# Optimization experiments

Hardware: AMD Instinct MI355X
Metric: run time of the kernel (lower is better)

## Reference

```python
import jax, jax.numpy as jnp
import numpy as np


def setup_inputs() -> dict:
    key = jax.random.key(0)
    ks = jax.random.split(key, 6)
    B, S, H = 4, 256, 768            # batch, subword seq len, BERT hidden
    N = 128                          # token_num (word-level units)
    HID, L = 1024, 16                # MLP hidden, label count
    all_hidden = jax.random.normal(ks[0], (B, S, H), dtype=jnp.float32)
    starts = jax.random.randint(ks[1], (B, N), 0, S)
    W1 = jax.random.normal(ks[2], (4 * H, HID), dtype=jnp.float32) * 0.02
    b1 = jnp.zeros((HID,), dtype=jnp.float32)
    W2 = jax.random.normal(ks[3], (HID, L), dtype=jnp.float32) * 0.02
    b2 = jnp.zeros((L,), dtype=jnp.float32)
    return {"all_hidden": all_hidden, "starts": starts,
            "W1": W1, "b1": b1, "W2": W2, "b2": b2}


def reference(all_hidden, starts, W1, b1, W2, b2):
    # Span gather: con_repr[b, n, :] = all_hidden[b, starts[b, n], :]
    con = jnp.take_along_axis(all_hidden, starts[:, :, None], axis=1)  # [B, N, H]
    B, N, H = con.shape
    a = jnp.broadcast_to(con[:, :, None, :], (B, N, N, H))  # ext_row
    c = jnp.broadcast_to(con[:, None, :, :], (B, N, N, H))  # ext_column
    table = jnp.concatenate([a, c, a - c, a * c], axis=-1)   # [B, N, N, 4H]
    hid = jnp.tanh(jnp.einsum('bijf,fh->bijh', table, W1) + b1)
    out = jnp.einsum('bijh,hl->bijl', hid, W2) + b2          # [B, N, N, L]
    return out
```

## Files before the change

kernel.cpp:

```cpp
#include <hip/hip_runtime.h>
#include <hip/hip_bf16.h>

typedef __attribute__((ext_vector_type(8))) short short8;
typedef __attribute__((ext_vector_type(8))) unsigned short ushort8;
typedef __attribute__((ext_vector_type(4))) float floatx4;
typedef __attribute__((ext_vector_type(16))) float floatx16;
typedef __attribute__((ext_vector_type(4))) unsigned int uint4v;
typedef __attribute__((ext_vector_type(2))) unsigned int uint2v;

#define DEVINL static __device__ __forceinline__

DEVINL float b2f(unsigned short s){ union{unsigned u; float f;} v; v.u=((unsigned)s)<<16; return v.f; }
DEVINL unsigned fbits(float f){ union{float f; unsigned u;} v; v.f=f; return v.u; }
DEVINL unsigned pack2(float f0, float f1){
  return __builtin_amdgcn_perm(fbits(f1)+0x8000u, fbits(f0)+0x8000u, 0x07060302u);
}
DEVINL unsigned cvt_pk(float lo, float hi){
  unsigned r;
  asm("v_cvt_pk_bf16_f32 %0, %1, %2" : "=v"(r) : "v"(lo), "v"(hi));
  return r;
}
DEVINL float tanh_fast(float v){
  float ex = __builtin_amdgcn_exp2f(v * 2.885390081777927f);
  return 1.f - 2.f*__builtin_amdgcn_rcpf(1.f + ex);
}

constexpr int Sc=256, Hc=768, Nc=128, HIDc=1024, Lc=16;

__global__ __launch_bounds__(256) void k_prep(const float* __restrict__ AH,
                                              const int* __restrict__ ST,
                                              const float* __restrict__ W1,
                                              const float* __restrict__ W2,
                                              unsigned short* __restrict__ con,
                                              unsigned short* __restrict__ w1mF,
                                              unsigned short* __restrict__ w2F2,
                                              unsigned short* __restrict__ wPQF){
  int bid = blockIdx.x, t = threadIdx.x;
  if (bid < 512) {
    int row = bid;
    int b = row >> 7;
    int st = ST[row];
    const float* src = AH + ((size_t)(b*Sc + st))*Hc;
    unsigned short* dst = con + (size_t)row*Hc;
    if (t < 192) {
      float4 v = reinterpret_cast<const float4*>(src)[t];
      uint2v o = { pack2(v.x, v.y), pack2(v.z, v.w) };
      *reinterpret_cast<uint2v*>(dst + 4*t) = o;
    }
  } else if (bid < 896) {
    int sid = (bid - 512)*256 + t;
    int l = sid & 63, kc = (sid >> 6) % 48, ht = sid / (48*64);
    int k = kc*16 + (l >> 5)*8;
    int h = ht*32 + (l & 31);
    const float* wp = W1 + (size_t)(2304 + k)*1024 + h;
    uint4v d;
    d[0] = pack2(wp[0],      wp[1024]);
    d[1] = pack2(wp[2*1024], wp[3*1024]);
    d[2] = pack2(wp[4*1024], wp[5*1024]);
    d[3] = pack2(wp[6*1024], wp[7*1024]);
    *reinterpret_cast<uint4v*>(w1mF + (size_t)sid*8) = d;
  } else if (bid < 912) {
    int gid = (bid - 896)*256 + t;
    int l = gid & 63, chunk = gid >> 6;
    int row = l & 31, s = l >> 5;
    unsigned u[4];
    #pragma unroll
    for (int p = 0; p < 4; ++p) {
      int e0 = 2*p, e1 = 2*p + 1;
      int h0 = chunk*16 + 4*s + (e0 & 3) + 8*(e0 >> 2);
      int h1 = chunk*16 + 4*s + (e1 & 3) + 8*(e1 >> 2);
      float v0 = (row < 16) ? W2[(size_t)h0*Lc + row] : 0.f;
      float v1 = (row < 16) ? W2[(size_t)h1*Lc + row] : 0.f;
      u[p] = pack2(v0, v1);
    }
    uint4v d = { u[0], u[1], u[2], u[3] };
    *reinterpret_cast<uint4v*>(w2F2 + (size_t)gid*8) = d;
  } else {
    int sid = (bid - 912)*256 + t;
    int lane = sid & 63, kcq = (sid >> 6) % 24, ht = sid / (24*64);
    int col = lane & 15, seg = lane >> 4;
    int hp = ht*16 + col;
    int kb = kcq*32 + seg*8;
    uint4v d;
    if (hp < 1024) {
      const float* w0 = W1 + (size_t)kb*1024 + hp;
      const float* wd = W1 + (size_t)(1536+kb)*1024 + hp;
      d[0] = pack2(w0[0]+wd[0],           w0[1024]+wd[1024]);
      d[1] = pack2(w0[2*1024]+wd[2*1024], w0[3*1024]+wd[3*1024]);
      d[2] = pack2(w0[4*1024]+wd[4*1024], w0[5*1024]+wd[5*1024]);
      d[3] = pack2(w0[6*1024]+wd[6*1024], w0[7*1024]+wd[7*1024]);
    } else {
      int hq = hp - 1024;
      const float* wc = W1 + (size_t)(768+kb)*1024 + hq;
      const float* wd = W1 + (size_t)(1536+kb)*1024 + hq;
      d[0] = pack2(wc[0]-wd[0],           wc[1024]-wd[1024]);
      d[1] = pack2(wc[2*1024]-wd[2*1024], wc[3*1024]-wd[3*1024]);
      d[2] = pack2(wc[4*1024]-wd[4*1024], wc[5*1024]-wd[5*1024]);
      d[3] = pack2(wc[6*1024]-wd[6*1024], wc[7*1024]-wd[7*1024]);
    }
    *reinterpret_cast<uint4v*>(wPQF + (size_t)sid*8) = d;
  }
}

__global__ __launch_bounds__(256) void k_pq(const unsigned short* __restrict__ con,
                                            const unsigned short* __restrict__ wPQF,
                                            float* __restrict__ P, float* __restrict__ Q){
  int rg = blockIdx.x >> 4, hg = blockIdx.x & 15;
  int t = threadIdx.x, w = t >> 6, lane = t & 63;
  int colh = lane & 15, rseg = lane >> 4;
  floatx4 zero = {0.f,0.f,0.f,0.f};
  floatx4 acc[2][2] = {{zero,zero},{zero,zero}};
  const unsigned short* a0p = con + (size_t)(rg*32 + colh)*Hc + rseg*8;
  const unsigned short* a1p = a0p + 16*Hc;
  const unsigned short* b0p = wPQF + (((size_t)((hg*8 + w*2)*24)) << 9) + (lane << 3);
  const unsigned short* b1p = b0p + (24 << 9);
  #pragma unroll
  for (int kc = 0; kc < 24; ++kc) {
    short8 af0 = *reinterpret_cast<const short8*>(a0p + kc*32);
    short8 af1 = *reinterpret_cast<const short8*>(a1p + kc*32);
    short8 bf0 = *reinterpret_cast<const short8*>(b0p + ((size_t)kc << 9));
    short8 bf1 = *reinterpret_cast<const short8*>(b1p + ((size_t)kc << 9));
    acc[0][0] = __builtin_amdgcn_mfma_f32_16x16x32_bf16(af0, bf0, acc[0][0], 0,0,0);
    acc[0][1] = __builtin_amdgcn_mfma_f32_16x16x32_bf16(af0, bf1, acc[0][1], 0,0,0);
    acc[1][0] = __builtin_amdgcn_mfma_f32_16x16x32_bf16(af1, bf0, acc[1][0], 0,0,0);
    acc[1][1] = __builtin_amdgcn_mfma_f32_16x16x32_bf16(af1, bf1, acc[1][1], 0,0,0);
  }
  #pragma unroll
  for (int m = 0; m < 2; ++m)
    #pragma unroll
    for (int n = 0; n < 2; ++n)
      #pragma unroll
      for (int rr = 0; rr < 4; ++rr) {
        int row = rg*32 + m*16 + rseg*4 + rr;
        int hp = hg*128 + w*32 + n*16 + colh;
        float val = acc[m][n][rr];
        if (hg < 8) P[(size_t)row*HIDc + hp] = val;
        else        Q[(size_t)row*HIDc + (hp - 1024)] = val;
      }
}

__global__ __launch_bounds__(512, 2) void k_main(const unsigned short* __restrict__ con,
    const unsigned short* __restrict__ w1mF, const unsigned short* __restrict__ w2F2,
    const float* __restrict__ P, const float* __restrict__ Q, const float* __restrict__ b1,
    const float* __restrict__ b2v, float* __restrict__ out){
  __shared__ __align__(16) unsigned short conF[2*48*64*8];
  __shared__ float Pi_lds[1024];

  int bid = blockIdx.x;
  int xcd = bid & 7, i = bid >> 3;
  int b = xcd >> 1, jh = xcd & 1;
  int bi = b*128 + i, bN = b*128;
  int t = threadIdx.x, w = t >> 6, lane = t & 63;
  int col32 = lane & 31, hi5 = lane >> 5;

  if (t < 256) {
    float4 p4 = reinterpret_cast<const float4*>(P + (size_t)(bN + i)*HIDc)[t];
    float4 b4 = reinterpret_cast<const float4*>(b1)[t];
    float4 s4 = { p4.x + b4.x, p4.y + b4.y, p4.z + b4.z, p4.w + b4.w };
    *reinterpret_cast<float4*>(&Pi_lds[4*t]) = s4;
  }
  {
    const unsigned short* conI = con + (size_t)(bN + i)*Hc;
    #pragma unroll
    for (int r = 0; r < 12; ++r) {
      int s = r*512 + t;
      int jt = (s >= 3072) ? 1 : 0;
      int rem = s - jt*3072;
      int kc = rem >> 6, ln = rem & 63;
      int j = jh*64 + jt*32 + (ln & 31);
      int kb = kc*16 + ((ln >> 5) << 3);
      ushort8 c8 = *reinterpret_cast<const ushort8*>(con + (size_t)(bN + j)*Hc + kb);
      ushort8 a8 = *reinterpret_cast<const ushort8*>(conI + kb);
      uint4v d;
      d[0] = cvt_pk(b2f(a8[0])*b2f(c8[0]), b2f(a8[1])*b2f(c8[1]));
      d[1] = cvt_pk(b2f(a8[2])*b2f(c8[2]), b2f(a8[3])*b2f(c8[3]));
      d[2] = cvt_pk(b2f(a8[4])*b2f(c8[4]), b2f(a8[5])*b2f(c8[5]));
      d[3] = cvt_pk(b2f(a8[6])*b2f(c8[6]), b2f(a8[7])*b2f(c8[7]));
      *reinterpret_cast<uint4v*>(conF + (size_t)s*8) = d;
    }
  }
  __syncthreads();

  const unsigned short* wp = w1mF + (((size_t)(w*4)*48) << 9) + (lane << 3);
  const unsigned short* yb = conF + (lane << 3);
  constexpr size_t HTS = (size_t)48 << 9;
  constexpr size_t KCS = (size_t)1 << 9;
  constexpr size_t JTS = (size_t)48 << 9;

  floatx16 a0j0, a0j1, a1j0, a1j1, a2j0, a2j1, a3j0, a3j1;
  #pragma unroll
  for (int r = 0; r < 16; ++r) {
    a0j0[r]=0.f; a0j1[r]=0.f; a1j0[r]=0.f; a1j1[r]=0.f;
    a2j0[r]=0.f; a2j1[r]=0.f; a3j0[r]=0.f; a3j1[r]=0.f;
  }

#define LOADSET(W0,W1,W2,W3,Y0,Y1, KC) { \
  W0 = *reinterpret_cast<const ushort8*>(wp + (0*HTS) + (size_t)(KC)*KCS); \
  W1 = *reinterpret_cast<const ushort8*>(wp + (1*HTS) + (size_t)(KC)*KCS); \
  W2 = *reinterpret_cast<const ushort8*>(wp + (2*HTS) + (size_t)(KC)*KCS); \
  W3 = *reinterpret_cast<const ushort8*>(wp + (3*HTS) + (size_t)(KC)*KCS); \
  Y0 = *reinterpret_cast<const short8*>(yb + (size_t)(KC)*KCS); \
  Y1 = *reinterpret_cast<const short8*>(yb + JTS + (size_t)(KC)*KCS); }

#define MFMA8S(W0,W1,W2,W3,Y0,Y1) { \
  a0j0 = __builtin_amdgcn_mfma_f32_32x32x16_bf16(W0, Y0, a0j0, 0,0,0); \
  a0j1 = __builtin_amdgcn_mfma_f32_32x32x16_bf16(W0, Y1, a0j1, 0,0,0); \
  a1j0 = __builtin_amdgcn_mfma_f32_32x32x16_bf16(W1, Y0, a1j0, 0,0,0); \
  a1j1 = __builtin_amdgcn_mfma_f32_32x32x16_bf16(W1, Y1, a1j1, 0,0,0); \
  a2j0 = __builtin_amdgcn_mfma_f32_32x32x16_bf16(W2, Y0, a2j0, 0,0,0); \
  a2j1 = __builtin_amdgcn_mfma_f32_32x32x16_bf16(W2, Y1, a2j1, 0,0,0); \
  a3j0 = __builtin_amdgcn_mfma_f32_32x32x16_bf16(W3, Y0, a3j0, 0,0,0); \
  a3j1 = __builtin_amdgcn_mfma_f32_32x32x16_bf16(W3, Y1, a3j1, 0,0,0); }

  {
    ushort8 wA0,wA1,wA2,wA3, wB0,wB1,wB2,wB3;
    short8 yA0,yA1, yB0,yB1;
    LOADSET(wA0,wA1,wA2,wA3,yA0,yA1, 0);
    #pragma unroll
    for (int kp = 0; kp < 24; ++kp) {
      LOADSET(wB0,wB1,wB2,wB3,yB0,yB1, 2*kp+1);
      MFMA8S(wA0,wA1,wA2,wA3,yA0,yA1);
      if (kp < 23) LOADSET(wA0,wA1,wA2,wA3,yA0,yA1, 2*kp+2);
      MFMA8S(wB0,wB1,wB2,wB3,yB0,yB1);
    }
  }
#undef LOADSET
#undef MFMA8S

  floatx16 acc2_0, acc2_1;
  #pragma unroll
  for (int r = 0; r < 16; ++r) { acc2_0[r] = 0.f; acc2_1[r] = 0.f; }

#define EPI(M, AJ0, AJ1) { \
  int htg = w*4 + (M); \
  const unsigned short* w2p = w2F2 + (((size_t)(htg*2)) << 9) + (lane << 3); \
  ushort8 wf0 = *reinterpret_cast<const ushort8*>(w2p); \
  ushort8 wf1 = *reinterpret_cast<const ushort8*>(w2p + 512); \
  int hbase = htg*32 + 4*hi5; \
  _Pragma("unroll") \
  for (int jt = 0; jt < 2; ++jt) { \
    const floatx16& a = (jt==0) ? AJ0 : AJ1; \
    floatx16& a2 = (jt==0) ? acc2_0 : acc2_1; \
    const float* qrow = Q + (size_t)(bN + jh*64 + jt*32 + col32)*HIDc + hbase; \
    unsigned hfu[2][4]; \
    _Pragma("unroll") \
    for (int q = 0; q < 4; ++q) { \
      floatx4 qv = *reinterpret_cast<const floatx4*>(qrow + 8*q); \
      floatx4 pf = *reinterpret_cast<const floatx4*>(&Pi_lds[hbase + 8*q]); \
      float t0 = tanh_fast(a[q*4+0] + pf[0] + qv[0]); \
      float t1 = tanh_fast(a[q*4+1] + pf[1] + qv[1]); \
      float t2 = tanh_fast(a[q*4+2] + pf[2] + qv[2]); \
      float t3 = tanh_fast(a[q*4+3] + pf[3] + qv[3]); \
      hfu[q >> 1][(q & 1)*2 + 0] = cvt_pk(t0, t1); \
      hfu[q >> 1][(q & 1)*2 + 1] = cvt_pk(t2, t3); \
    } \
    union { uint4v u; short8 s; } f0, f1; \
    f0.u[0]=hfu[0][0]; f0.u[1]=hfu[0][1]; f0.u[2]=hfu[0][2]; f0.u[3]=hfu[0][3]; \
    f1.u[0]=hfu[1][0]; f1.u[1]=hfu[1][1]; f1.u[2]=hfu[1][2]; f1.u[3]=hfu[1][3]; \
    a2 = __builtin_amdgcn_mfma_f32_32x32x16_bf16(wf0, f0.s, a2, 0,0,0); \
    a2 = __builtin_amdgcn_mfma_f32_32x32x16_bf16(wf1, f1.s, a2, 0,0,0); \
  } }

  EPI(0, a0j0, a0j1);
  EPI(1, a1j0, a1j1);
  EPI(2, a2j0, a2j1);
  EPI(3, a3j0, a3j1);
#undef EPI

  __syncthreads();
  float* red = reinterpret_cast<float*>(conF);
  #pragma unroll
  for (int q = 0; q < 2; ++q) {
    floatx4 v0 = { acc2_0[q*4+0], acc2_0[q*4+1], acc2_0[q*4+2], acc2_0[q*4+3] };
    floatx4 v1 = { acc2_1[q*4+0], acc2_1[q*4+1], acc2_1[q*4+2], acc2_1[q*4+3] };
    *reinterpret_cast<floatx4*>(&red[((w*4 + 0*2 + q)*64 + lane)*4]) = v0;
    *reinterpret_cast<floatx4*>(&red[((w*4 + 1*2 + q)*64 + lane)*4]) = v1;
  }
  __syncthreads();
  if (w < 4) {
    int jtR = w & 1, qR = w >> 1;
    floatx4 s = {0.f,0.f,0.f,0.f};
    #pragma unroll
    for (int src = 0; src < 8; ++src) {
      floatx4 v = *reinterpret_cast<const floatx4*>(&red[((src*4 + jtR*2 + qR)*64 + lane)*4]);
      s[0]+=v[0]; s[1]+=v[1]; s[2]+=v[2]; s[3]+=v[3];
    }
    int jout = jh*64 + jtR*32 + col32;
    int Lb = 8*qR + 4*hi5;
    float* op = out + ((size_t)bi*Nc + jout)*Lc + Lb;
    #pragma unroll
    for (int c = 0; c < 4; ++c) op[c] = s[c] + b2v[Lb + c];
  }
}

extern "C" void kernel_launch(void* const* d_in, const int* in_sizes, int n_in,
                              void* d_out, int out_size, void* d_ws, size_t ws_size,
                              hipStream_t stream) {
  const float* AH = (const float*)d_in[0];
  const int*   ST = (const int*)d_in[1];
  const float* W1 = (const float*)d_in[2];
  const float* b1 = (const float*)d_in[3];
  const float* W2 = (const float*)d_in[4];
  const float* b2 = (const float*)d_in[5];
  float* out = (float*)d_out;

  char* ws = (char*)d_ws;
  unsigned short* con  = (unsigned short*)ws;
  unsigned short* w1mF = (unsigned short*)(ws +   786432);
  unsigned short* wPQF = (unsigned short*)(ws +  2359296);
  float* P = (float*)(ws + 5505024);
  float* Q = (float*)(ws + 7602176);
  unsigned short* w2F2 = (unsigned short*)(ws + 9699328);

  k_prep<<<1680, 256, 0, stream>>>(AH, ST, W1, W2, con, w1mF, w2F2, wPQF);
  k_pq<<<256, 256, 0, stream>>>(con, wPQF, P, Q);
  k_main<<<1024, 512, 0, stream>>>(con, w1mF, w2F2, P, Q, b1, b2, out);
}
```

Baseline: 151.7 us.

## Stream W1 tiles into LDS via async global_load_lds double buffering

Replaces the register-prefetched global loads of the W1 fragments in the main GEMM loop with direct global-to-LDS async loads into a per-wave double-buffered LDS ring, gated by vmcnt waits and setprio around the MFMA block. The bias b1 is folded into P inside k_pq, so k_main no longer stages P+b1 into LDS and instead reads P directly from global in the epilogue. This aims to free VGPRs and overlap weight fetch with MFMA work, at the cost of extra LDS (about 64KB more per block, which may lower occupancy) and global reads of P in the epilogue.

```diff
diff --git a/kernel.cpp b/kernel.cpp
--- a/kernel.cpp
+++ b/kernel.cpp
@@ -23,6 +23,11 @@
 DEVINL float tanh_fast(float v){
   float ex = __builtin_amdgcn_exp2f(v * 2.885390081777927f);
   return 1.f - 2.f*__builtin_amdgcn_rcpf(1.f + ex);
+}
+DEVINL void gload_lds16(const void* g, void* l){
+  __builtin_amdgcn_global_load_lds(
+    (const __attribute__((address_space(1))) unsigned int*)g,
+    (__attribute__((address_space(3))) unsigned int*)l, 16, 0, 0);
 }
 
 constexpr int Sc=256, Hc=768, Nc=128, HIDc=1024, Lc=16;
@@ -104,7 +109,8 @@
 
 __global__ __launch_bounds__(256) void k_pq(const unsigned short* __restrict__ con,
                                             const unsigned short* __restrict__ wPQF,
-                                            float* __restrict__ P, float* __restrict__ Q){
+                                            const float* __restrict__ b1,
+                                            float* __restrict__ Pb, float* __restrict__ Q){
   int rg = blockIdx.x >> 4, hg = blockIdx.x & 15;
   int t = threadIdx.x, w = t >> 6, lane = t & 63;
   int colh = lane & 15, rseg = lane >> 4;
@@ -134,17 +140,17 @@
         int row = rg*32 + m*16 + rseg*4 + rr;
         int hp = hg*128 + w*32 + n*16 + colh;
         float val = acc[m][n][rr];
-        if (hg < 8) P[(size_t)row*HIDc + hp] = val;
+        if (hg < 8) Pb[(size_t)row*HIDc + hp] = val + b1[hp];
         else        Q[(size_t)row*HIDc + (hp - 1024)] = val;
       }
 }
 
 __global__ __launch_bounds__(512, 2) void k_main(const unsigned short* __restrict__ con,
     const unsigned short* __restrict__ w1mF, const unsigned short* __restrict__ w2F2,
-    const float* __restrict__ P, const float* __restrict__ Q, const float* __restrict__ b1,
+    const float* __restrict__ Pb, const float* __restrict__ Q,
     const float* __restrict__ b2v, float* __restrict__ out){
   __shared__ __align__(16) unsigned short conF[2*48*64*8];
-  __shared__ float Pi_lds[1024];
+  __shared__ __align__(16) unsigned short wxR[8][2][4][64][8];
 
   int bid = blockIdx.x;
   int xcd = bid & 7, i = bid >> 3;
@@ -153,12 +159,6 @@
   int t = threadIdx.x, w = t >> 6, lane = t & 63;
   int col32 = lane & 31, hi5 = lane >> 5;
 
-  if (t < 256) {
-    float4 p4 = reinterpret_cast<const float4*>(P + (size_t)(bN + i)*HIDc)[t];
-    float4 b4 = reinterpret_cast<const float4*>(b1)[t];
-    float4 s4 = { p4.x + b4.x, p4.y + b4.y, p4.z + b4.z, p4.w + b4.w };
-    *reinterpret_cast<float4*>(&Pi_lds[4*t]) = s4;
-  }
   {
     const unsigned short* conI = con + (size_t)(bN + i)*Hc;
     #pragma unroll
@@ -181,9 +181,7 @@
   }
   __syncthreads();
 
-  const unsigned short* wp = w1mF + (((size_t)(w*4)*48) << 9) + (lane << 3);
   const unsigned short* yb = conF + (lane << 3);
-  constexpr size_t HTS = (size_t)48 << 9;
   constexpr size_t KCS = (size_t)1 << 9;
   constexpr size_t JTS = (size_t)48 << 9;
 
@@ -194,42 +192,47 @@
     a2j0[r]=0.f; a2j1[r]=0.f; a3j0[r]=0.f; a3j1[r]=0.f;
   }
 
-#define LOADSET(W0,W1,W2,W3,Y0,Y1, KC) { \
-  W0 = *reinterpret_cast<const ushort8*>(wp + (0*HTS) + (size_t)(KC)*KCS); \
-  W1 = *reinterpret_cast<const ushort8*>(wp + (1*HTS) + (size_t)(KC)*KCS); \
-  W2 = *reinterpret_cast<const ushort8*>(wp + (2*HTS) + (size_t)(KC)*KCS); \
-  W3 = *reinterpret_cast<const ushort8*>(wp + (3*HTS) + (size_t)(KC)*KCS); \
-  Y0 = *reinterpret_cast<const short8*>(yb + (size_t)(KC)*KCS); \
-  Y1 = *reinterpret_cast<const short8*>(yb + JTS + (size_t)(KC)*KCS); }
-
-#define MFMA8S(W0,W1,W2,W3,Y0,Y1) { \
-  a0j0 = __builtin_amdgcn_mfma_f32_32x32x16_bf16(W0, Y0, a0j0, 0,0,0); \
-  a0j1 = __builtin_amdgcn_mfma_f32_32x32x16_bf16(W0, Y1, a0j1, 0,0,0); \
-  a1j0 = __builtin_amdgcn_mfma_f32_32x32x16_bf16(W1, Y0, a1j0, 0,0,0); \
-  a1j1 = __builtin_amdgcn_mfma_f32_32x32x16_bf16(W1, Y1, a1j1, 0,0,0); \
-  a2j0 = __builtin_amdgcn_mfma_f32_32x32x16_bf16(W2, Y0, a2j0, 0,0,0); \
-  a2j1 = __builtin_amdgcn_mfma_f32_32x32x16_bf16(W2, Y1, a2j1, 0,0,0); \
-  a3j0 = __builtin_amdgcn_mfma_f32_32x32x16_bf16(W3, Y0, a3j0, 0,0,0); \
-  a3j1 = __builtin_amdgcn_mfma_f32_32x32x16_bf16(W3, Y1, a3j1, 0,0,0); }
-
-  {
-    ushort8 wA0,wA1,wA2,wA3, wB0,wB1,wB2,wB3;
-    short8 yA0,yA1, yB0,yB1;
-    LOADSET(wA0,wA1,wA2,wA3,yA0,yA1, 0);
-    #pragma unroll
-    for (int kp = 0; kp < 24; ++kp) {
-      LOADSET(wB0,wB1,wB2,wB3,yB0,yB1, 2*kp+1);
-      MFMA8S(wA0,wA1,wA2,wA3,yA0,yA1);
-      if (kp < 23) LOADSET(wA0,wA1,wA2,wA3,yA0,yA1, 2*kp+2);
-      MFMA8S(wB0,wB1,wB2,wB3,yB0,yB1);
-    }
-  }
-#undef LOADSET
-#undef MFMA8S
+#define STAGE(S, SLOT) { \
+  _Pragma("unroll") \
+  for (int ht_ = 0; ht_ < 4; ++ht_) { \
+    const unsigned short* g_ = w1mF + (((size_t)((w*4 + ht_)*48 + (S))) << 9) + (lane << 3); \
+    gload_lds16(g_, &wxR[w][SLOT][ht_][0][0]); \
+  } }
+
+  STAGE(0, 0);
+  STAGE(1, 1);
+
+  #pragma unroll
+  for (int s = 0; s < 48; ++s) {
+    if (s < 47) { asm volatile("s_waitcnt vmcnt(4)" ::: "memory"); }
+    else        { asm volatile("s_waitcnt vmcnt(0)" ::: "memory"); }
+    __builtin_amdgcn_sched_barrier(0);
+    const int slot = s & 1;
+    short8 x0 = *reinterpret_cast<const short8*>(&wxR[w][slot][0][lane][0]);
+    short8 x1 = *reinterpret_cast<const short8*>(&wxR[w][slot][1][lane][0]);
+    short8 x2 = *reinterpret_cast<const short8*>(&wxR[w][slot][2][lane][0]);
+    short8 x3 = *reinterpret_cast<const short8*>(&wxR[w][slot][3][lane][0]);
+    short8 y0 = *reinterpret_cast<const short8*>(yb + (size_t)s*KCS);
+    short8 y1 = *reinterpret_cast<const short8*>(yb + JTS + (size_t)s*KCS);
+    __builtin_amdgcn_s_setprio(1);
+    a0j0 = __builtin_amdgcn_mfma_f32_32x32x16_bf16(x0, y0, a0j0, 0,0,0);
+    a0j1 = __builtin_amdgcn_mfma_f32_32x32x16_bf16(x0, y1, a0j1, 0,0,0);
+    a1j0 = __builtin_amdgcn_mfma_f32_32x32x16_bf16(x1, y0, a1j0, 0,0,0);
+    a1j1 = __builtin_amdgcn_mfma_f32_32x32x16_bf16(x1, y1, a1j1, 0,0,0);
+    a2j0 = __builtin_amdgcn_mfma_f32_32x32x16_bf16(x2, y0, a2j0, 0,0,0);
+    a2j1 = __builtin_amdgcn_mfma_f32_32x32x16_bf16(x2, y1, a2j1, 0,0,0);
+    a3j0 = __builtin_amdgcn_mfma_f32_32x32x16_bf16(x3, y0, a3j0, 0,0,0);
+    a3j1 = __builtin_amdgcn_mfma_f32_32x32x16_bf16(x3, y1, a3j1, 0,0,0);
+    __builtin_amdgcn_s_setprio(0);
+    __builtin_amdgcn_sched_barrier(0);
+    if (s < 46) STAGE(s + 2, slot);
+  }
+#undef STAGE
 
   floatx16 acc2_0, acc2_1;
   #pragma unroll
   for (int r = 0; r < 16; ++r) { acc2_0[r] = 0.f; acc2_1[r] = 0.f; }
+  const float* PbI = Pb + (size_t)(bN + i)*HIDc;
 
 #define EPI(M, AJ0, AJ1) { \
   int htg = w*4 + (M); \
@@ -246,7 +249,7 @@
     _Pragma("unroll") \
     for (int q = 0; q < 4; ++q) { \
       floatx4 qv = *reinterpret_cast<const floatx4*>(qrow + 8*q); \
-      floatx4 pf = *reinterpret_cast<const floatx4*>(&Pi_lds[hbase + 8*q]); \
+      floatx4 pf = *reinterpret_cast<const floatx4*>(PbI + hbase + 8*q); \
       float t0 = tanh_fast(a[q*4+0] + pf[0] + qv[0]); \
       float t1 = tanh_fast(a[q*4+1] + pf[1] + qv[1]); \
       float t2 = tanh_fast(a[q*4+2] + pf[2] + qv[2]); \
@@ -308,11 +311,11 @@
   unsigned short* con  = (unsigned short*)ws;
   unsigned short* w1mF = (unsigned short*)(ws +   786432);
   unsigned short* wPQF = (unsigned short*)(ws +  2359296);
-  float* P = (float*)(ws + 5505024);
-  float* Q = (float*)(ws + 7602176);
+  float* Pb = (float*)(ws + 5505024);
+  float* Q  = (float*)(ws + 7602176);
   unsigned short* w2F2 = (unsigned short*)(ws + 9699328);
 
   k_prep<<<1680, 256, 0, stream>>>(AH, ST, W1, W2, con, w1mF, w2F2, wPQF);
-  k_pq<<<256, 256, 0, stream>>>(con, wPQF, P, Q);
-  k_main<<<1024, 512, 0, stream>>>(con, w1mF, w2F2, P, Q, b1, b2, out);
-}
+  k_pq<<<256, 256, 0, stream>>>(con, wPQF, b1, Pb, Q);
+  k_main<<<1024, 512, 0, stream>>>(con, w1mF, w2F2, Pb, Q, b2, out);
+}
```

New measurement: 162.8 us. 7.4% more time.
